# Kernel tuning notes

Measured on AMD Instinct MI355X. Metric: run time of the kernel, lower is better.

## Reference

```python
import jax, jax.numpy as jnp
import numpy as np

N_NODES = 50000
N_EDGES = 800000
IN_DIM = 128
HID_DIM = 128
NUM_GRAPHS = 64


def gcn_conv(x, edge_index, W, b):
    """PyG GCNConv: symmetric-normalized aggregation with self-loops.
    out = D^{-1/2} (A + I) D^{-1/2} (x @ W) + b
    """
    n = x.shape[0]
    loop = jnp.arange(n, dtype=edge_index.dtype)
    src = jnp.concatenate([edge_index[0], loop])  # [E+N]
    dst = jnp.concatenate([edge_index[1], loop])
    deg = jax.ops.segment_sum(jnp.ones_like(dst, x.dtype), dst, num_segments=n)
    dinv = jnp.where(deg > 0, jax.lax.rsqrt(deg), 0.0)
    norm = dinv[src] * dinv[dst]  # [E+N]
    h = x @ W  # [N, H] transform before propagate (PyG order)
    msg = h[src] * norm[:, None]  # [E+N, H] gathered+scaled messages
    out = jax.ops.segment_sum(msg, dst, num_segments=n)  # scatter-add
    return out + b


def global_mean_pool(x, batch, num_graphs):
    s = jax.ops.segment_sum(x, batch, num_segments=num_graphs)
    cnt = jax.ops.segment_sum(jnp.ones((x.shape[0],), x.dtype), batch, num_segments=num_graphs)
    return s / jnp.maximum(cnt, 1.0)[:, None]


def setup_inputs() -> dict:
    key = jax.random.key(0)
    ks = jax.random.split(key, 8)
    x = jax.random.normal(ks[0], (N_NODES, IN_DIM), dtype=jnp.float32)
    edge_index = jax.random.randint(ks[1], (2, N_EDGES), 0, N_NODES, dtype=jnp.int64)
    batch = jnp.sort(jax.random.randint(ks[2], (N_NODES,), 0, NUM_GRAPHS, dtype=jnp.int64))
    s1 = 1.0 / np.sqrt(IN_DIM)
    s2 = 1.0 / np.sqrt(HID_DIM)
    W1 = jax.random.uniform(ks[3], (IN_DIM, HID_DIM), jnp.float32, -s1, s1)
    b1 = jnp.zeros((HID_DIM,), jnp.float32)
    W2 = jax.random.uniform(ks[4], (HID_DIM, HID_DIM), jnp.float32, -s2, s2)
    b2 = jnp.zeros((HID_DIM,), jnp.float32)
    Wc = jax.random.uniform(ks[5], (HID_DIM, 1), jnp.float32, -s2, s2)
    bc = jnp.zeros((1,), jnp.float32)
    return {"x": x, "edge_index": edge_index, "batch": batch,
            "W1": W1, "b1": b1, "W2": W2, "b2": b2, "Wc": Wc, "bc": bc}


def reference(x, edge_index, batch, W1, b1, W2, b2, Wc, bc):
    h = jax.nn.relu(gcn_conv(x, edge_index, W1, b1))
    # dropout p=0.1 is identity in eval mode
    h = gcn_conv(h, edge_index, W2, b2)
    g = global_mean_pool(h, batch, NUM_GRAPHS)  # [G, H]
    return jax.nn.sigmoid(g @ Wc + bc)  # [G, 1]
```

## Files before the change

### kernel.cpp

```cpp
#include <hip/hip_runtime.h>
#include <hip/hip_bf16.h>
#include <hip/hip_fp16.h>

#define N_NODES 50000
#define N_EDGES 800000
#define DIM     128
#define NG      64
#define GN      16
#define CAP     48
#define AGG_EB  256
#define LAXP    136

#define NBIN    196
#define SORT_B  250
#define EPB     3200

#define CAST_B  1563
#define VB_B    129
#define WF_B    8

typedef float  f2_t  __attribute__((ext_vector_type(2)));
typedef float  f32x4 __attribute__((ext_vector_type(4)));
typedef _Float16 f16x8 __attribute__((ext_vector_type(8)));
typedef _Float16 f16x4 __attribute__((ext_vector_type(4)));

__global__ void k_prep(const int* __restrict__ ei, int* __restrict__ binCnt,
                       const float4* __restrict__ x4, uint4* __restrict__ xq4,
                       const float* __restrict__ W2, const float* __restrict__ Wc,
                       const float* __restrict__ b2, float* __restrict__ v,
                       float* __restrict__ beta2,
                       const float* __restrict__ W1, f16x8* __restrict__ w1f) {
    __shared__ float red[4];
    __shared__ int hist[256];
    int bid = blockIdx.x, t = threadIdx.x;
    if (bid < SORT_B) {
        hist[t] = 0;
        __syncthreads();
        int base = bid * EPB;
        for (int r = 0; r < 13; r++) {
            int idx = r * 256 + t;
            if (idx < EPB) {
                int d = ei[N_EDGES + base + idx];
                atomicAdd(&hist[d >> 8], 1);
            }
        }
        __syncthreads();
        if (t < NBIN && hist[t] > 0) atomicAdd(&binCnt[t], hist[t]);
    } else if (bid < SORT_B + CAST_B) {
        int idx = (bid - SORT_B) * 256 + t;
        if (idx < N_NODES * DIM / 16) {
            uint4 o;
            unsigned* op = (unsigned*)&o;
            #pragma unroll
            for (int q = 0; q < 4; q++) {
                float4 f = x4[idx * 4 + q];
                int p = 0;
                p = __builtin_amdgcn_cvt_pk_fp8_f32(f.x, f.y, p, false);
                p = __builtin_amdgcn_cvt_pk_fp8_f32(f.z, f.w, p, true);
                op[q] = (unsigned)p;
            }
            xq4[idx] = o;
        }
    } else if (bid < SORT_B + CAST_B + VB_B) {
        int b = bid - (SORT_B + CAST_B);
        float p = 0.f;
        if (t < DIM) p = (b < DIM) ? W2[b * DIM + t] * Wc[t] : b2[t] * Wc[t];
        #pragma unroll
        for (int off = 32; off > 0; off >>= 1) p += __shfl_down(p, off, 64);
        if ((t & 63) == 0) red[t >> 6] = p;
        __syncthreads();
        if (t == 0) {
            float s = red[0] + red[1];
            if (b < DIM) v[b] = s; else beta2[0] = s;
        }
    } else {
        int idx = (bid - (SORT_B + CAST_B + VB_B)) * 256 + t;
        int ntile = idx >> 8, kb = (idx >> 6) & 3, l = idx & 63;
        int kbase = kb * 32 + (l >> 4) * 8;
        int n = ntile * 16 + (l & 15);
        f16x8 o;
        #pragma unroll
        for (int j = 0; j < 8; j++) o[j] = (_Float16)W1[(kbase + j) * DIM + n];
        w1f[idx] = o;
    }
}

__global__ void k_scan(const int* __restrict__ binCnt, int* __restrict__ binOff,
                       int* __restrict__ binCur) {
    __shared__ int s[256];
    int t = threadIdx.x;
    int c = (t < NBIN) ? binCnt[t] : 0;
    s[t] = c;
    #pragma unroll
    for (int off = 1; off < 256; off <<= 1) {
        __syncthreads();
        int v2 = (t >= off) ? s[t - off] : 0;
        __syncthreads();
        s[t] += v2;
    }
    __syncthreads();
    if (t < NBIN) {
        int excl = s[t] - c;
        binOff[t] = excl;
        binCur[t] = excl;
    }
}

__global__ void k_scatter(const int* __restrict__ ei, int* __restrict__ binCur,
                          unsigned int* __restrict__ sorted) {
    __shared__ int hist[256];
    __shared__ int cur[256];
    int bid = blockIdx.x, t = threadIdx.x;
    hist[t] = 0;
    __syncthreads();
    int base = bid * EPB;
    for (int r = 0; r < 13; r++) {
        int idx = r * 256 + t;
        if (idx < EPB) {
            int d = ei[N_EDGES + base + idx];
            atomicAdd(&hist[d >> 8], 1);
        }
    }
    __syncthreads();
    if (t < NBIN && hist[t] > 0) cur[t] = atomicAdd(&binCur[t], hist[t]);
    __syncthreads();
    for (int r = 0; r < 13; r++) {
        int idx = r * 256 + t;
        if (idx < EPB) {
            int e = base + idx;
            int s = ei[e];
            int d = ei[N_EDGES + e];
            int pos = atomicAdd(&cur[d >> 8], 1);
            sorted[pos] = (unsigned)s | ((unsigned)(d & 255) << 16);
        }
    }
}

__global__ void k_deg(const unsigned int* __restrict__ sorted,
                      const int* __restrict__ binOff, int* __restrict__ deg) {
    __shared__ int cnt[256];
    int b = blockIdx.x, t = threadIdx.x;
    cnt[t] = 0;
    __syncthreads();
    int lo = binOff[b];
    int hi = (b == NBIN - 1) ? N_EDGES : binOff[b + 1];
    for (int i = lo + t; i < hi; i += 256)
        atomicAdd(&cnt[sorted[i] >> 16], 1);
    __syncthreads();
    int node = b * 256 + t;
    if (node < N_NODES) deg[node] = cnt[t];
}

__global__ void k_build(const unsigned int* __restrict__ sorted,
                        const int* __restrict__ binOff, const int* __restrict__ deg,
                        unsigned int* __restrict__ csr) {
    __shared__ int cur[256];
    int b = blockIdx.x, t = threadIdx.x;
    cur[t] = 0;
    __syncthreads();
    int lo = binOff[b];
    int hi = (b == NBIN - 1) ? N_EDGES : binOff[b + 1];
    for (int i = lo + t; i < hi; i += 256) {
        unsigned e = sorted[i];
        unsigned src = e & 0xFFFFu;
        unsigned dLow = e >> 16;
        int pos = atomicAdd(&cur[dLow], 1);
        if (pos < CAP) {
            float w = rsqrtf((float)deg[src] + 1.f);
            unsigned hw = (unsigned)__half_as_ushort(__float2half(w));
            csr[(b * 256 + dLow) * CAP + pos] = src | (hw << 16);
        }
    }
}

__global__ __launch_bounds__(512) void k_node(
    const unsigned int* __restrict__ xq,
    const unsigned int* __restrict__ csr,
    const f16x8* __restrict__ w1f,
    const float* __restrict__ b1,
    const float* __restrict__ v, const int* __restrict__ deg,
    float* __restrict__ z2) {
    __shared__ _Float16 laxh[GN * LAXP];
    __shared__ float redm[GN * 8];
    int tid = threadIdx.x;
    int w = tid >> 6, l = tid & 63;
    int half = l >> 5, hl = l & 31;
    int node0 = blockIdx.x * GN;

    {
        int i = node0 + 2 * w + half;
        int start = i * CAP;
        int len = min(deg[i], CAP);
        int lm1 = (len > 0) ? len - 1 : 0;
        float di = rsqrtf((float)deg[i] + 1.f);

        unsigned su = xq[(size_t)i * 32 + hl];
        f2_t s01 = __builtin_amdgcn_cvt_pk_f32_fp8((int)su, false);
        f2_t s23 = __builtin_amdgcn_cvt_pk_f32_fp8((int)su, true);
        float a0 = di * s01.x, a1 = di * s01.y;
        float a2 = di * s23.x, a3 = di * s23.y;
        float b0 = 0.f, b1_ = 0.f, b2_ = 0.f, b3 = 0.f;
        float c0 = 0.f, c1 = 0.f, c2 = 0.f, c3 = 0.f;
        float d0 = 0.f, d1 = 0.f, d2 = 0.f, d3 = 0.f;

        int lenmax = max(len, __shfl_xor(len, 32, 64));
        for (int j = 0; j < lenmax; j += 4) {
            int j0 = min(j + 0, lm1), j1 = min(j + 1, lm1);
            int j2 = min(j + 2, lm1), j3 = min(j + 3, lm1);
            unsigned p0 = csr[start + j0];
            unsigned p1 = csr[start + j1];
            unsigned p2 = csr[start + j2];
            unsigned p3 = csr[start + j3];
            float w0 = (j + 0 < len) ? __half2float(__ushort_as_half((unsigned short)(p0 >> 16))) : 0.f;
            float w1 = (j + 1 < len) ? __half2float(__ushort_as_half((unsigned short)(p1 >> 16))) : 0.f;
            float w2 = (j + 2 < len) ? __half2float(__ushort_as_half((unsigned short)(p2 >> 16))) : 0.f;
            float w3 = (j + 3 < len) ? __half2float(__ushort_as_half((unsigned short)(p3 >> 16))) : 0.f;
            unsigned q0 = xq[(size_t)(p0 & 0xFFFFu) * 32 + hl];
            unsigned q1 = xq[(size_t)(p1 & 0xFFFFu) * 32 + hl];
            unsigned q2 = xq[(size_t)(p2 & 0xFFFFu) * 32 + hl];
            unsigned q3 = xq[(size_t)(p3 & 0xFFFFu) * 32 + hl];
            f2_t e01, e23;
            e01 = __builtin_amdgcn_cvt_pk_f32_fp8((int)q0, false);
            e23 = __builtin_amdgcn_cvt_pk_f32_fp8((int)q0, true);
            a0 = fmaf(w0, e01.x, a0); a1 = fmaf(w0, e01.y, a1);
            a2 = fmaf(w0, e23.x, a2); a3 = fmaf(w0, e23.y, a3);
            e01 = __builtin_amdgcn_cvt_pk_f32_fp8((int)q1, false);
            e23 = __builtin_amdgcn_cvt_pk_f32_fp8((int)q1, true);
            b0 = fmaf(w1, e01.x, b0); b1_ = fmaf(w1, e01.y, b1_);
            b2_ = fmaf(w1, e23.x, b2_); b3 = fmaf(w1, e23.y, b3);
            e01 = __builtin_amdgcn_cvt_pk_f32_fp8((int)q2, false);
            e23 = __builtin_amdgcn_cvt_pk_f32_fp8((int)q2, true);
            c0 = fmaf(w2, e01.x, c0); c1 = fmaf(w2, e01.y, c1);
            c2 = fmaf(w2, e23.x, c2); c3 = fmaf(w2, e23.y, c3);
            e01 = __builtin_amdgcn_cvt_pk_f32_fp8((int)q3, false);
            e23 = __builtin_amdgcn_cvt_pk_f32_fp8((int)q3, true);
            d0 = fmaf(w3, e01.x, d0); d1 = fmaf(w3, e01.y, d1);
            d2 = fmaf(w3, e23.x, d2); d3 = fmaf(w3, e23.y, d3);
        }
        a0 += b0 + c0 + d0; a1 += b1_ + c1 + d1;
        a2 += b2_ + c2 + d2; a3 += b3 + c3 + d3;
        f16x4 pk;
        pk[0] = (_Float16)(di * a0); pk[1] = (_Float16)(di * a1);
        pk[2] = (_Float16)(di * a2); pk[3] = (_Float16)(di * a3);
        *(f16x4*)&laxh[(2 * w + half) * LAXP + 4 * hl] = pk;
    }
    __syncthreads();

    f32x4 acc = {0.f, 0.f, 0.f, 0.f};
    #pragma unroll
    for (int kb = 0; kb < 4; kb++) {
        f16x8 af = *(const f16x8*)&laxh[(l & 15) * LAXP + kb * 32 + (l >> 4) * 8];
        f16x8 bf = w1f[(w * 4 + kb) * 64 + l];
        acc = __builtin_amdgcn_mfma_f32_16x16x32_f16(af, bf, acc, 0, 0, 0);
    }
    int n = w * 16 + (l & 15);
    float bn = b1[n], vn = v[n];
    #pragma unroll
    for (int r = 0; r < 4; r++) {
        float p = fmaxf(acc[r] + bn, 0.f) * vn;
        p += __shfl_xor(p, 1, 64);
        p += __shfl_xor(p, 2, 64);
        p += __shfl_xor(p, 4, 64);
        p += __shfl_xor(p, 8, 64);
        if ((l & 15) == 0) redm[((l >> 4) * 4 + r) * 8 + w] = p;
    }
    __syncthreads();
    if (tid < GN) {
        float s = 0.f;
        #pragma unroll
        for (int q = 0; q < 8; q++) s += redm[tid * 8 + q];
        z2[node0 + tid] = rsqrtf((float)deg[node0 + tid] + 1.f) * s;
    }
}

__global__ void k_aggz(const float* __restrict__ z2, const int* __restrict__ deg,
                       const int* __restrict__ ei, const int* __restrict__ batch,
                       float* __restrict__ gpartE, float* __restrict__ gpartN,
                       int* __restrict__ gcnt) {
    int bid = blockIdx.x, t = threadIdx.x;
    if (bid < AGG_EB) {
        __shared__ float bs[4][NG];
        bs[t >> 6][t & 63] = 0.f;
        __syncthreads();
        int wg = t >> 6;
        for (int base = bid * 1024; base < N_EDGES; base += AGG_EB * 1024) {
            #pragma unroll
            for (int k = 0; k < 4; k++) {
                int e = base + k * 256 + t;
                if (e < N_EDGES) {
                    int s = ei[e];
                    int d = ei[N_EDGES + e];
                    float dv = rsqrtf((float)deg[d] + 1.f);
                    atomicAdd(&bs[wg][batch[d]], dv * z2[s]);
                }
            }
        }
        __syncthreads();
        if (t < NG) gpartE[bid * NG + t] = bs[0][t] + bs[1][t] + bs[2][t] + bs[3][t];
    } else {
        __shared__ int range[2];
        __shared__ float rs[4];
        int g = bid - AGG_EB;
        if (t < 2) {
            int key = g + t;
            int lo = 0, hi = N_NODES;
            while (lo < hi) { int m = (lo + hi) >> 1; if (batch[m] < key) lo = m + 1; else hi = m; }
            range[t] = lo;
        }
        __syncthreads();
        int lo = range[0], hi = range[1];
        float loc = 0.f;
        for (int i = lo + t; i < hi; i += 256)
            loc += rsqrtf((float)deg[i] + 1.f) * z2[i];
        #pragma unroll
        for (int off = 32; off > 0; off >>= 1) loc += __shfl_down(loc, off, 64);
        if ((t & 63) == 0) rs[t >> 6] = loc;
        __syncthreads();
        if (t == 0) {
            gpartN[g] = rs[0] + rs[1] + rs[2] + rs[3];
            gcnt[g] = hi - lo;
        }
    }
}

__global__ void k_final(const float* __restrict__ gpartE, const float* __restrict__ gpartN,
                        const int* __restrict__ gcnt, const float* __restrict__ beta2,
                        const float* __restrict__ bcin, float* __restrict__ out) {
    __shared__ float acc[4][NG];
    int t = threadIdx.x;
    int g = t & 63, c = t >> 6;
    float s = 0.f;
    for (int k = 0; k < AGG_EB / 4; k++)
        s += gpartE[(c * (AGG_EB / 4) + k) * NG + g];
    acc[c][g] = s;
    __syncthreads();
    if (t < NG) {
        float tot = acc[0][t] + acc[1][t] + acc[2][t] + acc[3][t] + gpartN[t];
        int cnt = gcnt[t];
        float val = tot / (float)(cnt > 0 ? cnt : 1) + beta2[0] + bcin[0];
        out[t] = 1.f / (1.f + expf(-val));
    }
}

extern "C" void kernel_launch(void* const* d_in, const int* in_sizes, int n_in,
                              void* d_out, int out_size, void* d_ws, size_t ws_size,
                              hipStream_t stream) {
    const float* x   = (const float*)d_in[0];
    const int*   ei  = (const int*)  d_in[1];
    const int*   bat = (const int*)  d_in[2];
    const float* W1  = (const float*)d_in[3];
    const float* b1  = (const float*)d_in[4];
    const float* W2  = (const float*)d_in[5];
    const float* b2  = (const float*)d_in[6];
    const float* Wc  = (const float*)d_in[7];
    const float* bc  = (const float*)d_in[8];
    float* out = (float*)d_out;

    char* w = (char*)d_ws;
    size_t off = 0;
    auto alloc = [&](size_t bytes) -> void* {
        void* p = w + off;
        off = (off + bytes + 255) & ~(size_t)255;
        return p;
    };
    int*   binCnt  = (int*)  alloc(NBIN * 4);
    size_t zero_len = off;
    int*   binOff  = (int*)  alloc(NBIN * 4);
    int*   binCur  = (int*)  alloc(NBIN * 4);
    int*   deg     = (int*)  alloc(N_NODES * 4);
    float* z2      = (float*)alloc(N_NODES * 4);
    float* v       = (float*)alloc(DIM * 4);
    float* beta2   = (float*)alloc(4);
    float* gpartE  = (float*)alloc((size_t)AGG_EB * NG * 4);
    float* gpartN  = (float*)alloc(NG * 4);
    int*   gcnt    = (int*)  alloc(NG * 4);
    f16x8* w1f     = (f16x8*)alloc(2048 * 16);
    unsigned int* xq     = (unsigned int*)alloc((size_t)N_NODES * DIM);
    unsigned int* sorted = (unsigned int*)alloc((size_t)N_EDGES * 4);
    unsigned int* csr    = (unsigned int*)alloc((size_t)N_NODES * CAP * 4);
    (void)ws_size; (void)in_sizes; (void)n_in; (void)out_size;

    hipMemsetAsync(d_ws, 0, zero_len, stream);

    dim3 b256(256);
    k_prep<<<dim3(SORT_B + CAST_B + VB_B + WF_B), b256, 0, stream>>>(
        ei, binCnt, (const float4*)x, (uint4*)xq, W2, Wc, b2, v, beta2, W1, w1f);
    k_scan<<<dim3(1), b256, 0, stream>>>(binCnt, binOff, binCur);
    k_scatter<<<dim3(SORT_B), b256, 0, stream>>>(ei, binCur, sorted);
    k_deg<<<dim3(NBIN), b256, 0, stream>>>(sorted, binOff, deg);
    k_build<<<dim3(NBIN), b256, 0, stream>>>(sorted, binOff, deg, csr);
    k_node<<<dim3(N_NODES / GN), dim3(512), 0, stream>>>(
        xq, csr, w1f, b1, v, deg, z2);
    k_aggz<<<dim3(AGG_EB + NG), b256, 0, stream>>>(z2, deg, ei, bat, gpartE, gpartN, gcnt);
    k_final<<<dim3(1), b256, 0, stream>>>(gpartE, gpartN, gcnt, beta2, bc, out);
}
```

Measured before the change: 172.3 us.

## Fuse bin scan into scatter and widen CSR gather to 8-way vector loads

Removes the single-block scan kernel by having every scatter block redundantly compute the prefix sum of bin counts, saving one launch and a serialization point. binCur is now zeroed by the memset and offset by the locally computed exclusive scan. The node aggregation loop now loads CSR entries with two 128-bit loads per 8 neighbors and issues 8 independent gathers with 8 accumulator sets for more memory-level parallelism. Padding slots are no longer clamped, so unused CSR entries are read and their gathers may touch arbitrary rows, relying on zero weights.

```diff
diff --git a/kernel.cpp b/kernel.cpp
--- a/kernel.cpp
+++ b/kernel.cpp
@@ -85,32 +85,25 @@
     }
 }
 
-__global__ void k_scan(const int* __restrict__ binCnt, int* __restrict__ binOff,
-                       int* __restrict__ binCur) {
-    __shared__ int s[256];
-    int t = threadIdx.x;
-    int c = (t < NBIN) ? binCnt[t] : 0;
-    s[t] = c;
-    #pragma unroll
-    for (int off = 1; off < 256; off <<= 1) {
-        __syncthreads();
-        int v2 = (t >= off) ? s[t - off] : 0;
-        __syncthreads();
-        s[t] += v2;
-    }
-    __syncthreads();
-    if (t < NBIN) {
-        int excl = s[t] - c;
-        binOff[t] = excl;
-        binCur[t] = excl;
-    }
-}
-
-__global__ void k_scatter(const int* __restrict__ ei, int* __restrict__ binCur,
+__global__ void k_scatter(const int* __restrict__ ei, const int* __restrict__ binCnt,
+                          int* __restrict__ binCur, int* __restrict__ binOff,
                           unsigned int* __restrict__ sorted) {
+    __shared__ int soff[256];
     __shared__ int hist[256];
     __shared__ int cur[256];
     int bid = blockIdx.x, t = threadIdx.x;
+    int c = (t < NBIN) ? binCnt[t] : 0;
+    soff[t] = c;
+    #pragma unroll
+    for (int o = 1; o < 256; o <<= 1) {
+        __syncthreads();
+        int v2 = (t >= o) ? soff[t - o] : 0;
+        __syncthreads();
+        soff[t] += v2;
+    }
+    __syncthreads();
+    int excl = soff[t] - c;
+    if (bid == 0 && t < NBIN) binOff[t] = excl;
     hist[t] = 0;
     __syncthreads();
     int base = bid * EPB;
@@ -122,7 +115,7 @@
         }
     }
     __syncthreads();
-    if (t < NBIN && hist[t] > 0) cur[t] = atomicAdd(&binCur[t], hist[t]);
+    if (t < NBIN && hist[t] > 0) cur[t] = excl + atomicAdd(&binCur[t], hist[t]);
     __syncthreads();
     for (int r = 0; r < 13; r++) {
         int idx = r * 256 + t;
@@ -189,56 +182,48 @@
 
     {
         int i = node0 + 2 * w + half;
-        int start = i * CAP;
         int len = min(deg[i], CAP);
-        int lm1 = (len > 0) ? len - 1 : 0;
         float di = rsqrtf((float)deg[i] + 1.f);
 
         unsigned su = xq[(size_t)i * 32 + hl];
         f2_t s01 = __builtin_amdgcn_cvt_pk_f32_fp8((int)su, false);
         f2_t s23 = __builtin_amdgcn_cvt_pk_f32_fp8((int)su, true);
-        float a0 = di * s01.x, a1 = di * s01.y;
-        float a2 = di * s23.x, a3 = di * s23.y;
-        float b0 = 0.f, b1_ = 0.f, b2_ = 0.f, b3 = 0.f;
-        float c0 = 0.f, c1 = 0.f, c2 = 0.f, c3 = 0.f;
-        float d0 = 0.f, d1 = 0.f, d2 = 0.f, d3 = 0.f;
+        float ax[8], ay[8], az[8], aw[8];
+        #pragma unroll
+        for (int k = 0; k < 8; k++) { ax[k] = 0.f; ay[k] = 0.f; az[k] = 0.f; aw[k] = 0.f; }
+        ax[0] = di * s01.x; ay[0] = di * s01.y;
+        az[0] = di * s23.x; aw[0] = di * s23.y;
 
         int lenmax = max(len, __shfl_xor(len, 32, 64));
-        for (int j = 0; j < lenmax; j += 4) {
-            int j0 = min(j + 0, lm1), j1 = min(j + 1, lm1);
-            int j2 = min(j + 2, lm1), j3 = min(j + 3, lm1);
-            unsigned p0 = csr[start + j0];
-            unsigned p1 = csr[start + j1];
-            unsigned p2 = csr[start + j2];
-            unsigned p3 = csr[start + j3];
-            float w0 = (j + 0 < len) ? __half2float(__ushort_as_half((unsigned short)(p0 >> 16))) : 0.f;
-            float w1 = (j + 1 < len) ? __half2float(__ushort_as_half((unsigned short)(p1 >> 16))) : 0.f;
-            float w2 = (j + 2 < len) ? __half2float(__ushort_as_half((unsigned short)(p2 >> 16))) : 0.f;
-            float w3 = (j + 3 < len) ? __half2float(__ushort_as_half((unsigned short)(p3 >> 16))) : 0.f;
-            unsigned q0 = xq[(size_t)(p0 & 0xFFFFu) * 32 + hl];
-            unsigned q1 = xq[(size_t)(p1 & 0xFFFFu) * 32 + hl];
-            unsigned q2 = xq[(size_t)(p2 & 0xFFFFu) * 32 + hl];
-            unsigned q3 = xq[(size_t)(p3 & 0xFFFFu) * 32 + hl];
-            f2_t e01, e23;
-            e01 = __builtin_amdgcn_cvt_pk_f32_fp8((int)q0, false);
-            e23 = __builtin_amdgcn_cvt_pk_f32_fp8((int)q0, true);
-            a0 = fmaf(w0, e01.x, a0); a1 = fmaf(w0, e01.y, a1);
-            a2 = fmaf(w0, e23.x, a2); a3 = fmaf(w0, e23.y, a3);
-            e01 = __builtin_amdgcn_cvt_pk_f32_fp8((int)q1, false);
-            e23 = __builtin_amdgcn_cvt_pk_f32_fp8((int)q1, true);
-            b0 = fmaf(w1, e01.x, b0); b1_ = fmaf(w1, e01.y, b1_);
-            b2_ = fmaf(w1, e23.x, b2_); b3 = fmaf(w1, e23.y, b3);
-            e01 = __builtin_amdgcn_cvt_pk_f32_fp8((int)q2, false);
-            e23 = __builtin_amdgcn_cvt_pk_f32_fp8((int)q2, true);
-            c0 = fmaf(w2, e01.x, c0); c1 = fmaf(w2, e01.y, c1);
-            c2 = fmaf(w2, e23.x, c2); c3 = fmaf(w2, e23.y, c3);
-            e01 = __builtin_amdgcn_cvt_pk_f32_fp8((int)q3, false);
-            e23 = __builtin_amdgcn_cvt_pk_f32_fp8((int)q3, true);
-            d0 = fmaf(w3, e01.x, d0); d1 = fmaf(w3, e01.y, d1);
-            d2 = fmaf(w3, e23.x, d2); d3 = fmaf(w3, e23.y, d3);
-        }
-        a0 += b0 + c0 + d0; a1 += b1_ + c1 + d1;
-        a2 += b2_ + c2 + d2; a3 += b3 + c3 + d3;
+        int lmp = (lenmax + 7) & ~7;
+        const uint4* csr4 = (const uint4*)csr;
+        int base4 = i * (CAP / 4);
+        for (int j = 0; j < lmp; j += 8) {
+            uint4 ca = csr4[base4 + (j >> 2)];
+            uint4 cb = csr4[base4 + (j >> 2) + 1];
+            unsigned pe[8] = {ca.x, ca.y, ca.z, ca.w, cb.x, cb.y, cb.z, cb.w};
+            unsigned q[8];
+            #pragma unroll
+            for (int k = 0; k < 8; k++)
+                q[k] = xq[(size_t)(pe[k] & 0xFFFFu) * 32 + hl];
+            float wgt[8];
+            #pragma unroll
+            for (int k = 0; k < 8; k++)
+                wgt[k] = (j + k < len)
+                    ? __half2float(__ushort_as_half((unsigned short)(pe[k] >> 16))) : 0.f;
+            #pragma unroll
+            for (int k = 0; k < 8; k++) {
+                f2_t e01 = __builtin_amdgcn_cvt_pk_f32_fp8((int)q[k], false);
+                f2_t e23 = __builtin_amdgcn_cvt_pk_f32_fp8((int)q[k], true);
+                ax[k] = fmaf(wgt[k], e01.x, ax[k]);
+                ay[k] = fmaf(wgt[k], e01.y, ay[k]);
+                az[k] = fmaf(wgt[k], e23.x, az[k]);
+                aw[k] = fmaf(wgt[k], e23.y, aw[k]);
+            }
+        }
+        float a0 = 0.f, a1 = 0.f, a2 = 0.f, a3 = 0.f;
+        #pragma unroll
+        for (int k = 0; k < 8; k++) { a0 += ax[k]; a1 += ay[k]; a2 += az[k]; a3 += aw[k]; }
         f16x4 pk;
         pk[0] = (_Float16)(di * a0); pk[1] = (_Float16)(di * a1);
         pk[2] = (_Float16)(di * a2); pk[3] = (_Float16)(di * a3);
@@ -364,9 +349,9 @@
         return p;
     };
     int*   binCnt  = (int*)  alloc(NBIN * 4);
+    int*   binCur  = (int*)  alloc(NBIN * 4);
     size_t zero_len = off;
     int*   binOff  = (int*)  alloc(NBIN * 4);
-    int*   binCur  = (int*)  alloc(NBIN * 4);
     int*   deg     = (int*)  alloc(N_NODES * 4);
     float* z2      = (float*)alloc(N_NODES * 4);
     float* v       = (float*)alloc(DIM * 4);
@@ -385,8 +370,7 @@
     dim3 b256(256);
     k_prep<<<dim3(SORT_B + CAST_B + VB_B + WF_B), b256, 0, stream>>>(
         ei, binCnt, (const float4*)x, (uint4*)xq, W2, Wc, b2, v, beta2, W1, w1f);
-    k_scan<<<dim3(1), b256, 0, stream>>>(binCnt, binOff, binCur);
-    k_scatter<<<dim3(SORT_B), b256, 0, stream>>>(ei, binCur, sorted);
+    k_scatter<<<dim3(SORT_B), b256, 0, stream>>>(ei, binCnt, binCur, binOff, sorted);
     k_deg<<<dim3(NBIN), b256, 0, stream>>>(sorted, binOff, deg);
     k_build<<<dim3(NBIN), b256, 0, stream>>>(sorted, binOff, deg, csr);
     k_node<<<dim3(N_NODES / GN), dim3(512), 0, stream>>>(
```

Measured after the change: 167.8 us. 1.03x faster.
